# Optimization experiments

Measured on AMD Instinct MI355X. Metric: run time of the kernel, lower is better.

## Reference

```python
import jax, jax.numpy as jnp
import numpy as np

B, NQ, NV, DIM, HEADS, K = 2, 2048, 2048, 256, 8, 8
HD = DIM // HEADS
HID = 4 * DIM
SCALE = HD ** -0.5
EPS = 1e-5


def setup_inputs() -> dict:
    key = jax.random.key(0)
    ks = jax.random.split(key, 40)
    r = lambda i, s: jax.random.normal(ks[i], s, jnp.float32) * 0.02
    inp = {
        'q': jax.random.normal(ks[0], (B, NQ, DIM), jnp.float32),
        'v': jax.random.normal(ks[1], (B, NV, DIM), jnp.float32),
        'q_pos': jax.random.normal(ks[2], (B, NQ, 3), jnp.float32),
        'v_pos': jax.random.normal(ks[3], (B, NV, 3), jnp.float32),
        'self_knn_index': jax.random.randint(ks[4], (B, NQ, K), 0, NQ, jnp.int32),
        'cross_knn_index': jax.random.randint(ks[5], (B, NQ, K), 0, NV, jnp.int32),
        # LayerNorms (gamma=1, beta=0)
        'norm1_g': jnp.ones(DIM), 'norm1_b': jnp.zeros(DIM),
        'normq_g': jnp.ones(DIM), 'normq_b': jnp.zeros(DIM),
        'normv_g': jnp.ones(DIM), 'normv_b': jnp.zeros(DIM),
        'norm2_g': jnp.ones(DIM), 'norm2_b': jnp.zeros(DIM),
        # self-attention (qkv_bias=False), proj has bias
        'sa_qkv_w': r(6, (DIM, 3 * DIM)),
        'sa_proj_w': r(7, (DIM, DIM)), 'sa_proj_b': jnp.zeros(DIM),
        # cross-attention: q proj and kv proj (no bias), out proj with bias
        'ca_q_w': r(8, (DIM, DIM)),
        'ca_kv_w': r(9, (DIM, 2 * DIM)),
        'ca_proj_w': r(10, (DIM, DIM)), 'ca_proj_b': jnp.zeros(DIM),
        # MLP
        'fc1_w': r(11, (DIM, HID)), 'fc1_b': jnp.zeros(HID),
        'fc2_w': r(12, (HID, DIM)), 'fc2_b': jnp.zeros(DIM),
        # kNN maps
        'knn_w': r(13, (2 * DIM, DIM)), 'knn_b': jnp.zeros(DIM),
        'merge_w': r(14, (2 * DIM, DIM)), 'merge_b': jnp.zeros(DIM),
        'knnx_w': r(15, (2 * DIM, DIM)), 'knnx_b': jnp.zeros(DIM),
        'mergex_w': r(16, (2 * DIM, DIM)), 'mergex_b': jnp.zeros(DIM),
    }
    return inp


def _ln(x, g, b):
    m = x.mean(-1, keepdims=True)
    var = x.var(-1, keepdims=True)
    return (x - m) / jnp.sqrt(var + EPS) * g + b


def _heads(x):  # [B,N,DIM] -> [B,H,N,HD]
    Bx, N, _ = x.shape
    return x.reshape(Bx, N, HEADS, HD).transpose(0, 2, 1, 3)


def _attend(qh, kh, vh, proj_w, proj_b):
    a = jax.nn.softmax(jnp.einsum('bhqd,bhkd->bhqk', qh, kh) * SCALE, axis=-1)
    o = jnp.einsum('bhqk,bhkd->bhqd', a, vh)
    Bx, _, N, _ = o.shape
    o = o.transpose(0, 2, 1, 3).reshape(Bx, N, DIM)
    return o @ proj_w + proj_b


_gather = jax.vmap(lambda pts, idx: pts[idx])  # ([N,D],[Nq,K]) -> [Nq,K,D]


def _knn_feature(qn, vn, idx):  # gather -> diff/cat -> [B,Nq,K,2D]
    local = _gather(vn, idx)                      # [B,Nq,K,D]
    qe = qn[:, :, None, :]                        # [B,Nq,1,D]
    return jnp.concatenate([local - qe, jnp.broadcast_to(qe, local.shape)], -1)


def reference(q, v, q_pos, v_pos, self_knn_index, cross_knn_index,
              norm1_g, norm1_b, normq_g, normq_b, normv_g, normv_b,
              norm2_g, norm2_b, sa_qkv_w, sa_proj_w, sa_proj_b,
              ca_q_w, ca_kv_w, ca_proj_w, ca_proj_b,
              fc1_w, fc1_b, fc2_w, fc2_b,
              knn_w, knn_b, merge_w, merge_b,
              knnx_w, knnx_b, mergex_w, mergex_b):
    # ---- self-attention block with self-kNN branch ----
    nq = _ln(q, norm1_g, norm1_b)
    qkv = nq @ sa_qkv_w
    qh, kh, vh = (_heads(t) for t in jnp.split(qkv, 3, axis=-1))
    sa_out = _attend(qh, kh, vh, sa_proj_w, sa_proj_b)
    f = _knn_feature(nq, nq, self_knn_index)
    knn_out = jax.nn.leaky_relu(f @ knn_w + knn_b, 0.2).max(axis=-2)
    q1 = jnp.concatenate([sa_out, knn_out], -1) @ merge_w + merge_b
    q = q + q1
    # ---- cross-attention block with cross-kNN branch ----
    nq2 = _ln(q, normq_g, normq_b)
    nv = _ln(v, normv_g, normv_b)
    qh = _heads(nq2 @ ca_q_w)
    kh, vh = (_heads(t) for t in jnp.split(nv @ ca_kv_w, 2, axis=-1))
    ca_out = _attend(qh, kh, vh, ca_proj_w, ca_proj_b)
    f = _knn_feature(nq2, nv, cross_knn_index)
    knnx_out = jax.nn.leaky_relu(f @ knnx_w + knnx_b, 0.2).max(axis=-2)
    q2 = jnp.concatenate([ca_out, knnx_out], -1) @ mergex_w + mergex_b
    q = q + q2
    # ---- MLP block ----
    h = _ln(q, norm2_g, norm2_b)
    h = jax.nn.gelu(h @ fc1_w + fc1_b, approximate=False)
    q = q + (h @ fc2_w + fc2_b)
    return q
```

## Files before the change

### kernel.cpp

```cpp
#include <hip/hip_runtime.h>
#include <math.h>

#define NQC   2048
#define NKVC  2048
#define DIMC  256
#define SCALEF 0.2550348810731232f

typedef short bfrag __attribute__((ext_vector_type(8)));
typedef float ffrag __attribute__((ext_vector_type(4)));
typedef unsigned short us8 __attribute__((ext_vector_type(8)));

__device__ __forceinline__ float gelu_exact(float x) {
    return 0.5f * x * (1.0f + erff(x * 0.70710678118654752f));
}
__device__ __forceinline__ unsigned short f2bf(float f) {
    union { float f; unsigned u; } v; v.f = f;
    unsigned r = v.u + 0x7FFFu + ((v.u >> 16) & 1u);
    return (unsigned short)(r >> 16);
}
__device__ __forceinline__ float bf2f(unsigned short u) {
    union { unsigned u; float f; } v; v.u = ((unsigned)u) << 16;
    return v.f;
}
__device__ __forceinline__ float fexp2(float x) {
    float r; asm("v_exp_f32 %0, %1" : "=v"(r) : "v"(x)); return r;
}
__device__ __forceinline__ unsigned cvt_pk_bf16(float lo, float hi) {
    unsigned r; asm("v_cvt_pk_bf16_f32 %0, %1, %2" : "=v"(r) : "v"(lo), "v"(hi));
    return r;
}

__device__ __forceinline__ void ln_row(
    const float* __restrict__ x, const float* __restrict__ g,
    const float* __restrict__ b, unsigned short* __restrict__ y, int row)
{
    int lane = threadIdx.x & 63;
    const float* xr = x + (size_t)row * DIMC + lane * 4;
    float4 vv = *(const float4*)xr;
    float s  = vv.x + vv.y + vv.z + vv.w;
    float sq = vv.x*vv.x + vv.y*vv.y + vv.z*vv.z + vv.w*vv.w;
    #pragma unroll
    for (int off = 32; off >= 1; off >>= 1) {
        s  += __shfl_xor(s, off);
        sq += __shfl_xor(sq, off);
    }
    float mean = s * (1.0f/DIMC);
    float inv  = rsqrtf(sq * (1.0f/DIMC) - mean*mean + 1e-5f);
    float4 gg = *(const float4*)(g + lane*4);
    float4 bb = *(const float4*)(b + lane*4);
    ushort4 o;
    o.x = f2bf((vv.x - mean) * inv * gg.x + bb.x);
    o.y = f2bf((vv.y - mean) * inv * gg.y + bb.y);
    o.z = f2bf((vv.z - mean) * inv * gg.z + bb.z);
    o.w = f2bf((vv.w - mean) * inv * gg.w + bb.w);
    *(ushort4*)(y + (size_t)row * DIMC + lane * 4) = o;
}

__global__ __launch_bounds__(256) void prep_w(
    const float* __restrict__ qkv, const float* __restrict__ knn,
    const float* __restrict__ proj, const float* __restrict__ merge,
    const float* __restrict__ caq, const float* __restrict__ knnx,
    const float* __restrict__ cakv, const float* __restrict__ projx,
    const float* __restrict__ mergex, const float* __restrict__ fc1,
    const float* __restrict__ fc2, unsigned short* __restrict__ dst,
    const float* __restrict__ lx, const float* __restrict__ lg,
    const float* __restrict__ lb, unsigned short* __restrict__ ly,
    const float* __restrict__ vx, const float* __restrict__ vg,
    const float* __restrict__ vb, unsigned short* __restrict__ vy,
    const float* __restrict__ pb1, const float* __restrict__ mb1, float* __restrict__ bf1o,
    const float* __restrict__ pbx, const float* __restrict__ mbx, float* __restrict__ bfxo)
{
    __shared__ unsigned short T[64][72];
    int blk = blockIdx.x, tid = threadIdx.x;
    if (blk >= 2528) {
        const float* bp = (blk == 2528) ? pb1 : pbx;
        const float* Wm = (blk == 2528) ? merge : mergex;
        const float* bm = (blk == 2528) ? mb1 : mbx;
        float* o        = (blk == 2528) ? bf1o : bfxo;
        int m = tid;
        float acc = bm[m];
        for (int k = 0; k < 256; ++k) acc += bp[k] * Wm[(size_t)k * 256 + m];
        o[m] = acc;
        return;
    }
    if (blk >= 1504) {
        ln_row(vx, vg, vb, vy, (blk - 1504) * 4 + (tid >> 6));
        return;
    }
    if (blk >= 480) {
        ln_row(lx, lg, lb, ly, (blk - 480) * 4 + (tid >> 6));
        return;
    }
    if (blk >= 352) {
        int l = blk - 352;
        const float* s; unsigned short* d;
        if (l < 64) { s = proj;  d = dst + 327680; }
        else        { s = projx; d = dst + 851968; l -= 64; }
        int e = (l * 256 + tid) * 4;
        float4 v = *(const float4*)(s + e);
        ushort4 o;
        o.x = f2bf(v.x); o.y = f2bf(v.y); o.z = f2bf(v.z); o.w = f2bf(v.w);
        *(ushort4*)(d + e) = o;
        return;
    }
    int t = blk;
    const float* src; const float* src2 = nullptr; int sN;
    unsigned short* dp; int dK; float scale = 1.0f; int n0, k0;
    if (t < 48)       { src = qkv;          sN = 768;  dp = dst;           dK = 256;
                        n0 = (t % 12) * 64; k0 = (t / 12) * 64; if (n0 < 256) scale = SCALEF; }
    else if (t < 64)  { int u = t - 48;  src = knn;          sN = 256; dp = dst + 196608; dK = 256;
                        n0 = (u & 3) * 64; k0 = (u >> 2) * 64; }
    else if (t < 80)  { int u = t - 64;  src = knn + 65536;  src2 = knn; sN = 256; dp = dst + 262144; dK = 256;
                        n0 = (u & 3) * 64; k0 = (u >> 2) * 64; }
    else if (t < 112) { int u = t - 80;  src = merge;        sN = 256; dp = dst + 393216; dK = 512;
                        n0 = (u & 3) * 64; k0 = (u >> 2) * 64; }
    else if (t < 128) { int u = t - 112; src = caq;          sN = 256; dp = dst + 524288; dK = 256;
                        n0 = (u & 3) * 64; k0 = (u >> 2) * 64; scale = SCALEF; }
    else if (t < 144) { int u = t - 128; src = knnx + 65536; src2 = knnx; sN = 256; dp = dst + 589824; dK = 256;
                        n0 = (u & 3) * 64; k0 = (u >> 2) * 64; }
    else if (t < 176) { int u = t - 144; src = cakv;         sN = 512; dp = dst + 655360; dK = 256;
                        n0 = (u & 7) * 64; k0 = (u >> 3) * 64; }
    else if (t < 192) { int u = t - 176; src = knnx;         sN = 256; dp = dst + 786432; dK = 256;
                        n0 = (u & 3) * 64; k0 = (u >> 2) * 64; }
    else if (t < 224) { int u = t - 192; src = mergex;       sN = 256; dp = dst + 917504; dK = 512;
                        n0 = (u & 3) * 64; k0 = (u >> 2) * 64; }
    else if (t < 288) { int u = t - 224; src = fc1;          sN = 1024; dp = dst + 1048576; dK = 256;
                        n0 = (u & 15) * 64; k0 = (u >> 4) * 64; }
    else              { int u = t - 288; src = fc2;          sN = 256; dp = dst + 1310720; dK = 1024;
                        n0 = (u & 3) * 64; k0 = (u >> 2) * 64; }
    int r = tid >> 2, c0 = (tid & 3) * 16;
    float va[16];
    {
        const float* sp = src + (size_t)(k0 + r) * sN + n0 + c0;
        float4 f0 = *(const float4*)(sp);
        float4 f1 = *(const float4*)(sp + 4);
        float4 f2 = *(const float4*)(sp + 8);
        float4 f3 = *(const float4*)(sp + 12);
        va[0]=f0.x; va[1]=f0.y; va[2]=f0.z;  va[3]=f0.w;
        va[4]=f1.x; va[5]=f1.y; va[6]=f1.z;  va[7]=f1.w;
        va[8]=f2.x; va[9]=f2.y; va[10]=f2.z; va[11]=f2.w;
        va[12]=f3.x; va[13]=f3.y; va[14]=f3.z; va[15]=f3.w;
        if (src2) {
            const float* s2 = src2 + (size_t)(k0 + r) * sN + n0 + c0;
            float4 h0 = *(const float4*)(s2);
            float4 h1 = *(const float4*)(s2 + 4);
            float4 h2 = *(const float4*)(s2 + 8);
            float4 h3 = *(const float4*)(s2 + 12);
            va[0]-=h0.x; va[1]-=h0.y; va[2]-=h0.z;  va[3]-=h0.w;
            va[4]-=h1.x; va[5]-=h1.y; va[6]-=h1.z;  va[7]-=h1.w;
            va[8]-=h2.x; va[9]-=h2.y; va[10]-=h2.z; va[11]-=h2.w;
            va[12]-=h3.x; va[13]-=h3.y; va[14]-=h3.z; va[15]-=h3.w;
        }
    }
    #pragma unroll
    for (int i = 0; i < 16; ++i) T[c0 + i][r] = f2bf(va[i] * scale);
    __syncthreads();
    {
        int n = tid >> 2, kk = (tid & 3) * 16;
        unsigned short* d = dp + (size_t)(n0 + n) * dK + k0 + kk;
        *(us8*)d       = *(const us8*)&T[n][kk];
        *(us8*)(d + 8) = *(const us8*)&T[n][kk + 8];
    }
}

__global__ __launch_bounds__(256) void ln_b(
    const float* __restrict__ x, const float* __restrict__ g,
    const float* __restrict__ b, unsigned short* __restrict__ y)
{
    ln_row(x, g, b, y, blockIdx.x * 4 + (threadIdx.x >> 6));
}

template<int ACT, int RESID, int OUTBF>
__device__ __forceinline__ void gemm_body(
    const unsigned short* __restrict__ A, int lda,
    const unsigned short* __restrict__ Wt,
    const float* __restrict__ bias,
    const float* __restrict__ resid, int ldr,
    void* __restrict__ Cp, int ldc, int Kc, int row0, int col0,
    unsigned short (* __restrict__ Alds)[72],
    unsigned short (* __restrict__ Wlds)[72])
{
    const int tid = threadIdx.x;
    const int wid = tid >> 6, lane = tid & 63;
    const int lm = lane & 15, quad = lane >> 4;
    const int wr = wid >> 1, wc = wid & 1;
    const int ar = tid >> 2, ac = (tid & 3) * 16;
    const unsigned short* Ag = A  + (size_t)(row0 + ar) * lda + ac;
    const unsigned short* Wg = Wt + (size_t)(col0 + ar) * Kc  + ac;

    us8 a0 = *(const us8*)Ag;
    us8 a1 = *(const us8*)(Ag + 8);
    us8 w0 = *(const us8*)Wg;
    us8 w1 = *(const us8*)(Wg + 8);

    ffrag acc[2][2];
    #pragma unroll
    for (int mi = 0; mi < 2; ++mi)
        #pragma unroll
        for (int ni = 0; ni < 2; ++ni)
            acc[mi][ni] = (ffrag){0.f, 0.f, 0.f, 0.f};

    for (int k0 = 0;;) {
        __syncthreads();
        *(us8*)&Alds[ar][ac]   = a0;
        *(us8*)&Alds[ar][ac+8] = a1;
        *(us8*)&Wlds[ar][ac]   = w0;
        *(us8*)&Wlds[ar][ac+8] = w1;
        __syncthreads();
        k0 += 64;
        if (k0 < Kc) {
            a0 = *(const us8*)(Ag + k0);
            a1 = *(const us8*)(Ag + k0 + 8);
            w0 = *(const us8*)(Wg + k0);
            w1 = *(const us8*)(Wg + k0 + 8);
        }
        #pragma unroll
        for (int kc = 0; kc < 2; ++kc) {
            bfrag af[2], bw[2];
            #pragma unroll
            for (int mi = 0; mi < 2; ++mi)
                af[mi] = *(const bfrag*)&Alds[wr*32 + mi*16 + lm][kc*32 + quad*8];
            #pragma unroll
            for (int ni = 0; ni < 2; ++ni)
                bw[ni] = *(const bfrag*)&Wlds[wc*32 + ni*16 + lm][kc*32 + quad*8];
            #pragma unroll
            for (int mi = 0; mi < 2; ++mi)
                #pragma unroll
                for (int ni = 0; ni < 2; ++ni)
                    acc[mi][ni] = __builtin_amdgcn_mfma_f32_16x16x32_bf16(
                        af[mi], bw[ni], acc[mi][ni], 0, 0, 0);
        }
        if (k0 >= Kc) break;
    }
    #pragma unroll
    for (int mi = 0; mi < 2; ++mi) {
        #pragma unroll
        for (int ni = 0; ni < 2; ++ni) {
            int gr = row0 + wr*32 + mi*16 + quad*4;
            int gc = col0 + wc*32 + ni*16 + lm;
            float bv = bias ? bias[gc] : 0.f;
            #pragma unroll
            for (int r = 0; r < 4; ++r) {
                float o = acc[mi][ni][r] + bv;
                if (ACT == 1) o = gelu_exact(o);
                if (RESID) o += resid[(size_t)(gr + r) * ldr + gc];
                if (OUTBF) ((unsigned short*)Cp)[(size_t)(gr + r) * ldc + gc] = f2bf(o);
                else       ((float*)Cp)[(size_t)(gr + r) * ldc + gc] = o;
            }
        }
    }
}

template<int ACT, int RESID, int OUTBF>
__global__ __launch_bounds__(256) void gemm64(
    const unsigned short* __restrict__ A, int lda,
    const unsigned short* __restrict__ Wt,
    const float* __restrict__ bias,
    const float* __restrict__ resid, int ldr,
    void* __restrict__ Cp, int ldc, int Kc)
{
    __shared__ unsigned short Alds[64][72];
    __shared__ unsigned short Wlds[64][72];
    gemm_body<ACT,RESID,OUTBF>(A, lda, Wt, bias, resid, ldr, Cp, ldc, Kc,
                               blockIdx.y * 64, blockIdx.x * 64, Alds, Wlds);
}

__global__ __launch_bounds__(256) void gemm_qkv_fold(
    const unsigned short* __restrict__ XB, const unsigned short* __restrict__ WT1,
    unsigned short* __restrict__ A1,
    const unsigned short* __restrict__ WTmerge, const unsigned short* __restrict__ projbf,
    unsigned short* __restrict__ WTf1,
    const unsigned short* __restrict__ WTmergex, const unsigned short* __restrict__ projxbf,
    unsigned short* __restrict__ WTfx)
{
    __shared__ unsigned short Alds[64][72];
    __shared__ unsigned short Wlds[64][72];
    const unsigned short *A, *Wt; unsigned short* C;
    int lda, ldc, row0, col0;
    if (blockIdx.y >= 64) {
        if (blockIdx.x >= 16) return;
        row0 = (blockIdx.x >> 2) * 64; col0 = (blockIdx.x & 3) * 64;
        lda = 512; ldc = 256;
        if (blockIdx.y == 64) { A = WTmerge;  Wt = projbf;  C = WTf1; }
        else                  { A = WTmergex; Wt = projxbf; C = WTfx; }
    } else {
        A = XB; Wt = WT1; C = A1; lda = 256; ldc = 1280;
        row0 = blockIdx.y * 64; col0 = blockIdx.x * 64;
    }
    gemm_body<0,0,1>(A, lda, Wt, nullptr, nullptr, 0, C, ldc, 256, row0, col0, Alds, Wlds);
}

template<int ACT, int RESID, int OUTBF>
__global__ __launch_bounds__(512) void gemm64x8(
    const unsigned short* __restrict__ A, int lda,
    const unsigned short* __restrict__ Wt,
    const float* __restrict__ bias,
    const float* __restrict__ resid, int ldr,
    void* __restrict__ Cp, int ldc, int Kc)
{
    __shared__ unsigned short Alds[2][64][72];
    __shared__ unsigned short Wlds[2][64][72];
    __shared__ float Red[64][68];
    const int tid = threadIdx.x;
    const int g = tid >> 8;
    const int t = tid & 255;
    const int wid2 = (tid >> 6) & 3, lane = tid & 63;
    const int lm = lane & 15, quad = lane >> 4;
    const int wr = wid2 >> 1, wc = wid2 & 1;
    const int row0 = blockIdx.y * 64, col0 = blockIdx.x * 64;
    const int ar = t >> 2, ac = (t & 3) * 16;
    const int KH = Kc >> 1;
    const unsigned short* Ag = A  + (size_t)(row0 + ar) * lda + g * KH + ac;
    const unsigned short* Wg = Wt + (size_t)(col0 + ar) * Kc  + g * KH + ac;

    us8 a0 = *(const us8*)Ag;
    us8 a1 = *(const us8*)(Ag + 8);
    us8 w0 = *(const us8*)Wg;
    us8 w1 = *(const us8*)(Wg + 8);

    ffrag acc[2][2];
    #pragma unroll
    for (int mi = 0; mi < 2; ++mi)
        #pragma unroll
        for (int ni = 0; ni < 2; ++ni)
            acc[mi][ni] = (ffrag){0.f, 0.f, 0.f, 0.f};

    for (int k0 = 0;;) {
        __syncthreads();
        *(us8*)&Alds[g][ar][ac]   = a0;
        *(us8*)&Alds[g][ar][ac+8] = a1;
        *(us8*)&Wlds[g][ar][ac]   = w0;
        *(us8*)&Wlds[g][ar][ac+8] = w1;
        __syncthreads();
        k0 += 64;
        if (k0 < KH) {
            a0 = *(const us8*)(Ag + k0);
            a1 = *(const us8*)(Ag + k0 + 8);
            w0 = *(const us8*)(Wg + k0);
            w1 = *(const us8*)(Wg + k0 + 8);
        }
        #pragma unroll
        for (int kc = 0; kc < 2; ++kc) {
            bfrag af[2], bw[2];
            #pragma unroll
            for (int mi = 0; mi < 2; ++mi)
                af[mi] = *(const bfrag*)&Alds[g][wr*32 + mi*16 + lm][kc*32 + quad*8];
            #pragma unroll
            for (int ni = 0; ni < 2; ++ni)
                bw[ni] = *(const bfrag*)&Wlds[g][wc*32 + ni*16 + lm][kc*32 + quad*8];
            #pragma unroll
            for (int mi = 0; mi < 2; ++mi)
                #pragma unroll
                for (int ni = 0; ni < 2; ++ni)
                    acc[mi][ni] = __builtin_amdgcn_mfma_f32_16x16x32_bf16(
                        af[mi], bw[ni], acc[mi][ni], 0, 0, 0);
        }
        if (k0 >= KH) break;
    }
    __syncthreads();
    if (g == 1) {
        #pragma unroll
        for (int mi = 0; mi < 2; ++mi)
            #pragma unroll
            for (int ni = 0; ni < 2; ++ni) {
                int lr = wr*32 + mi*16 + quad*4;
                int lc = wc*32 + ni*16 + lm;
                #pragma unroll
                for (int r = 0; r < 4; ++r)
                    Red[lr + r][lc] = acc[mi][ni][r];
            }
    }
    __syncthreads();
    if (g == 0) {
        #pragma unroll
        for (int mi = 0; mi < 2; ++mi) {
            #pragma unroll
            for (int ni = 0; ni < 2; ++ni) {
                int lr = wr*32 + mi*16 + quad*4;
                int lc = wc*32 + ni*16 + lm;
                int gr = row0 + lr;
                int gc = col0 + lc;
                float bv = bias ? bias[gc] : 0.f;
                #pragma unroll
                for (int r = 0; r < 4; ++r) {
                    float o = acc[mi][ni][r] + Red[lr + r][lc] + bv;
                    if (ACT == 1) o = gelu_exact(o);
                    if (RESID) o += resid[(size_t)(gr + r) * ldr + gc];
                    if (OUTBF) ((unsigned short*)Cp)[(size_t)(gr + r) * ldc + gc] = f2bf(o);
                    else       ((float*)Cp)[(size_t)(gr + r) * ldc + gc] = o;
                }
            }
        }
    }
}

__global__ __launch_bounds__(512) void gemm64x8f(
    const unsigned short* __restrict__ Op, const float* __restrict__ Lp,
    const unsigned short* __restrict__ Akn,
    const unsigned short* __restrict__ Wat,
    const unsigned short* __restrict__ Wkn,
    const float* __restrict__ bias,
    const float* __restrict__ resid,
    float* __restrict__ Cp)
{
    __shared__ unsigned short Alds[2][64][72];
    __shared__ unsigned short Wlds[2][64][72];
    __shared__ float Red[64][68];
    const int tid = threadIdx.x;
    const int g = tid >> 8;
    const int t = tid & 255;
    const int wid2 = (tid >> 6) & 3, lane = tid & 63;
    const int lm = lane & 15, quad = lane >> 4;
    const int wr = wid2 >> 1, wc = wid2 & 1;
    const int row0 = blockIdx.y * 64, col0 = blockIdx.x * 64;
    const int ar = t >> 2, ac = (t & 3) * 16;
    const int grow = row0 + ar;

    const unsigned short* O0 = Op + (size_t)grow * 256 + ac;
    const unsigned short* O1 = Op + (size_t)(4096 + grow) * 256 + ac;
    const float* L0 = Lp + (size_t)grow * 8;
    const float* L1 = Lp + (size_t)(4096 + grow) * 8;
    const unsigned short* Ak = Akn + (size_t)grow * 512 + ac;
    const unsigned short* Wg = g ? Wkn + (size_t)(col0 + ar) * 512 + ac
                                 : Wat + (size_t)(col0 + ar) * 256 + ac;

    us8 a0, a1, o10, o11;
    float li = 0.f;
    if (g == 0) {
        a0  = *(const us8*)O0;  a1  = *(const us8*)(O0 + 8);
        o10 = *(const us8*)O1;  o11 = *(const us8*)(O1 + 8);
        li  = 1.0f / (L0[ac >> 5] + L1[ac >> 5]);
    } else {
        a0 = *(const us8*)Ak;   a1 = *(const us8*)(Ak + 8);
    }
    us8 w0 = *(const us8*)Wg;
    us8 w1 = *(const us8*)(Wg + 8);

    ffrag acc[2][2];
    #pragma unroll
    for (int mi = 0; mi < 2; ++mi)
        #pragma unroll
        for (int ni = 0; ni < 2; ++ni)
            acc[mi][ni] = (ffrag){0.f, 0.f, 0.f, 0.f};

    for (int k0 = 0;;) {
        us8 s0 = a0, s1 = a1;
        if (g == 0) {
            #pragma unroll
            for (int i = 0; i < 8; ++i) {
                s0[i] = f2bf((bf2f(a0[i]) + bf2f(o10[i])) * li);
                s1[i] = f2bf((bf2f(a1[i]) + bf2f(o11[i])) * li);
            }
        }
        __syncthreads();
        *(us8*)&Alds[g][ar][ac]   = s0;
        *(us8*)&Alds[g][ar][ac+8] = s1;
        *(us8*)&Wlds[g][ar][ac]   = w0;
        *(us8*)&Wlds[g][ar][ac+8] = w1;
        __syncthreads();
        k0 += 64;
        if (k0 < 256) {
            if (g == 0) {
                a0  = *(const us8*)(O0 + k0);  a1  = *(const us8*)(O0 + k0 + 8);
                o10 = *(const us8*)(O1 + k0);  o11 = *(const us8*)(O1 + k0 + 8);
                li  = 1.0f / (L0[(k0 + ac) >> 5] + L1[(k0 + ac) >> 5]);
            } else {
                a0 = *(const us8*)(Ak + k0);   a1 = *(const us8*)(Ak + k0 + 8);
            }
            w0 = *(const us8*)(Wg + k0);
            w1 = *(const us8*)(Wg + k0 + 8);
        }
        #pragma unroll
        for (int kc = 0; kc < 2; ++kc) {
            bfrag af[2], bw[2];
            #pragma unroll
            for (int mi = 0; mi < 2; ++mi)
                af[mi] = *(const bfrag*)&Alds[g][wr*32 + mi*16 + lm][kc*32 + quad*8];
            #pragma unroll
            for (int ni = 0; ni < 2; ++ni)
                bw[ni] = *(const bfrag*)&Wlds[g][wc*32 + ni*16 + lm][kc*32 + quad*8];
            #pragma unroll
            for (int mi = 0; mi < 2; ++mi)
                #pragma unroll
                for (int ni = 0; ni < 2; ++ni)
                    acc[mi][ni] = __builtin_amdgcn_mfma_f32_16x16x32_bf16(
                        af[mi], bw[ni], acc[mi][ni], 0, 0, 0);
        }
        if (k0 >= 256) break;
    }
    __syncthreads();
    if (g == 1) {
        #pragma unroll
        for (int mi = 0; mi < 2; ++mi)
            #pragma unroll
            for (int ni = 0; ni < 2; ++ni) {
                int lr = wr*32 + mi*16 + quad*4;
                int lc = wc*32 + ni*16 + lm;
                #pragma unroll
                for (int r = 0; r < 4; ++r)
                    Red[lr + r][lc] = acc[mi][ni][r];
            }
    }
    __syncthreads();
    if (g == 0) {
        #pragma unroll
        for (int mi = 0; mi < 2; ++mi) {
            #pragma unroll
            for (int ni = 0; ni < 2; ++ni) {
                int lr = wr*32 + mi*16 + quad*4;
                int lc = wc*32 + ni*16 + lm;
                int gr = row0 + lr;
                int gc = col0 + lc;
                float bv = bias[gc];
                #pragma unroll
                for (int r = 0; r < 4; ++r)
                    Cp[(size_t)(gr + r) * 256 + gc] =
                        acc[mi][ni][r] + Red[lr + r][lc] + bv
                        + resid[(size_t)(gr + r) * 256 + gc];
            }
        }
    }
}

__global__ __launch_bounds__(256) void gemm64_dual(
    const unsigned short* __restrict__ XB,
    const unsigned short* __restrict__ NVB,
    const unsigned short* __restrict__ WT2,
    const unsigned short* __restrict__ WT3,
    unsigned short* __restrict__ A2,
    unsigned short* __restrict__ A3)
{
    __shared__ unsigned short Alds[64][72];
    __shared__ unsigned short Wlds[64][72];
    const unsigned short* A; const unsigned short* Wt;
    unsigned short* C; int ldc, col0;
    if (blockIdx.x < 8) { A = XB;  Wt = WT2; C = A2; ldc = 512; col0 = blockIdx.x * 64; }
    else                { A = NVB; Wt = WT3; C = A3; ldc = 768; col0 = (blockIdx.x - 8) * 64; }
    gemm_body<0,0,1>(A, 256, Wt, nullptr, nullptr, 0, C, ldc, 256,
                     blockIdx.y * 64, col0, Alds, Wlds);
}

__global__ __launch_bounds__(256) void attn_gather(
    const unsigned short* __restrict__ Qp, int ldq,
    const unsigned short* __restrict__ Kp, int ldk,
    const unsigned short* __restrict__ Vp, int ldv,
    unsigned short* __restrict__ Op, float* __restrict__ Lp,
    const unsigned short* __restrict__ P, int ldp,
    const unsigned short* __restrict__ Base, int ldb,
    const float* __restrict__ gbias, const int* __restrict__ idx,
    unsigned short* __restrict__ gout, int ldgo)
{
    __shared__ unsigned short Klds[64][40];
    __shared__ __align__(16) unsigned short Vt[32][72];
    __shared__ __align__(16) unsigned short Plds[4][16][72];
    int tid = threadIdx.x, wid = tid >> 6, lane = tid & 63;

    if (blockIdx.z >= 4) {
        int gbid = blockIdx.x + 32 * (blockIdx.y + 8 * (blockIdx.z - 4));
        int q = gbid * 4 + wid;
        int b = q >> 11;
        int c = lane * 4;
        ushort4 bu = *(const ushort4*)(Base + (size_t)q * ldb + c);
        float4 bi = *(const float4*)(gbias + c);
        float bsx = bf2f(bu.x) + bi.x, bsy = bf2f(bu.y) + bi.y;
        float bsz = bf2f(bu.z) + bi.z, bsw = bf2f(bu.w) + bi.w;
        float4 acc = make_float4(-3e38f, -3e38f, -3e38f, -3e38f);
        const int* ip = idx + (size_t)q * 8;
        #pragma unroll
        for (int k = 0; k < 8; ++k) {
            int j = ip[k];
            ushort4 pu = *(const ushort4*)(P + ((size_t)(b * NKVC + j)) * ldp + c);
            float t;
            t = bsx + bf2f(pu.x); t = t > 0.f ? t : 0.2f * t; acc.x = fmaxf(acc.x, t);
            t = bsy + bf2f(pu.y); t = t > 0.f ? t : 0.2f * t; acc.y = fmaxf(acc.y, t);
            t = bsz + bf2f(pu.z); t = t > 0.f ? t : 0.2f * t; acc.z = fmaxf(acc.z, t);
            t = bsw + bf2f(pu.w); t = t > 0.f ? t : 0.2f * t; acc.w = fmaxf(acc.w, t);
        }
        ushort4 o;
        o.x = f2bf(acc.x); o.y = f2bf(acc.y); o.z = f2bf(acc.z); o.w = f2bf(acc.w);
        *(ushort4*)(gout + (size_t)q * ldgo + c) = o;
        return;
    }

    int zc = blockIdx.z, bb = zc >> 1, ck = zc & 1;
    int h = blockIdx.y;
    int hoff = h * 32;
    int lm = lane & 15, quad = lane >> 4;
    size_t qbase  = (size_t)bb * NQC;
    size_t kvbase = (size_t)bb * NKVC;
    int q0 = blockIdx.x * 64 + wid * 16;

    bfrag aq = *(const bfrag*)(Qp + (qbase + q0 + lm) * (size_t)ldq + hoff + quad * 8);

    float l_r[4] = {0.f, 0.f, 0.f, 0.f};
    ffrag oacc[2];
    oacc[0] = (ffrag){0.f, 0.f, 0.f, 0.f};
    oacc[1] = (ffrag){0.f, 0.f, 0.f, 0.f};

    const int kkey = tid >> 2, kd0 = (tid & 3) * 8;
    const int vkey = tid & 63, vd0 = (tid >> 6) * 8;
    const int vcol = ((vkey & 15) << 2) | (vkey >> 4);
    const unsigned short* kg0 = Kp + (kvbase + kkey) * (size_t)ldk + hoff + kd0;
    const unsigned short* vg0 = Vp + (kvbase + vkey) * (size_t)ldv + hoff + vd0;

    for (int kt = ck * 16; kt < ck * 16 + 16; ++kt) {
        us8 kv = *(const us8*)(kg0 + (size_t)kt * 64 * ldk);
        us8 vv = *(const us8*)(vg0 + (size_t)kt * 64 * ldv);
        __syncthreads();
        *(us8*)&Klds[kkey][kd0] = kv;
        #pragma unroll
        for (int i = 0; i < 8; ++i) Vt[vd0 + i][vcol] = vv[i];
        __syncthreads();

        ffrag sacc[4];
        #pragma unroll
        for (int t = 0; t < 4; ++t) {
            bfrag bk = *(const bfrag*)&Klds[t*16 + lm][quad * 8];
            sacc[t] = __builtin_amdgcn_mfma_f32_16x16x32_bf16(
                aq, bk, (ffrag){0.f,0.f,0.f,0.f}, 0, 0, 0);
        }

        #pragma unroll
        for (int r = 0; r < 4; ++r) {
            float p0 = fexp2(sacc[0][r]), p1 = fexp2(sacc[1][r]);
            float p2 = fexp2(sacc[2][r]), p3 = fexp2(sacc[3][r]);
            l_r[r] += (p0 + p1) + (p2 + p3);
            unsigned u0 = cvt_pk_bf16(p0, p1);
            unsigned u1 = cvt_pk_bf16(p2, p3);
            *(uint2*)&Plds[wid][quad*4 + r][lm << 2] = make_uint2(u0, u1);
        }
        asm volatile("s_waitcnt lgkmcnt(0)" ::: "memory");

        #pragma unroll
        for (int kc = 0; kc < 2; ++kc) {
            bfrag ap = *(const bfrag*)&Plds[wid][lm][kc*32 + quad*8];
            #pragma unroll
            for (int nt = 0; nt < 2; ++nt) {
                bfrag bv = *(const bfrag*)&Vt[nt*16 + lm][kc*32 + quad*8];
                oacc[nt] = __builtin_amdgcn_mfma_f32_16x16x32_bf16(
                    ap, bv, oacc[nt], 0, 0, 0);
            }
        }
    }
    #pragma unroll
    for (int nt = 0; nt < 2; ++nt)
        #pragma unroll
        for (int r = 0; r < 4; ++r)
            Op[((size_t)ck * 4096 + qbase + q0 + quad*4 + r) * 256 + hoff + nt*16 + lm]
                = f2bf(oacc[nt][r]);
    #pragma unroll
    for (int r = 0; r < 4; ++r) {
        float l = l_r[r];
        l += __shfl_xor(l, 1);
        l += __shfl_xor(l, 2);
        l += __shfl_xor(l, 4);
        l += __shfl_xor(l, 8);
        if (lm == 0)
            Lp[((size_t)ck * 4096 + qbase + q0 + quad*4 + r) * 8 + h] = l;
    }
}

extern "C" void kernel_launch(void* const* d_in, const int* in_sizes, int n_in,
                              void* d_out, int out_size, void* d_ws, size_t ws_size,
                              hipStream_t stream) {
    const float* q_in   = (const float*)d_in[0];
    const float* v_in   = (const float*)d_in[1];
    const int*   idx_s  = (const int*)d_in[4];
    const int*   idx_x  = (const int*)d_in[5];
    const float* n1g = (const float*)d_in[6],  *n1b = (const float*)d_in[7];
    const float* nqg = (const float*)d_in[8],  *nqb = (const float*)d_in[9];
    const float* nvg = (const float*)d_in[10], *nvb = (const float*)d_in[11];
    const float* n2g = (const float*)d_in[12], *n2b = (const float*)d_in[13];
    const float* sa_qkv_w  = (const float*)d_in[14];
    const float* sa_proj_w = (const float*)d_in[15];
    const float* sa_proj_b = (const float*)d_in[16];
    const float* ca_q_w    = (const float*)d_in[17];
    const float* ca_kv_w   = (const float*)d_in[18];
    const float* ca_proj_w = (const float*)d_in[19];
    const float* ca_proj_b = (const float*)d_in[20];
    const float* fc1_w = (const float*)d_in[21], *fc1_b = (const float*)d_in[22];
    const float* fc2_w = (const float*)d_in[23], *fc2_b = (const float*)d_in[24];
    const float* knn_w   = (const float*)d_in[25], *knn_b   = (const float*)d_in[26];
    const float* merge_w = (const float*)d_in[27], *merge_b = (const float*)d_in[28];
    const float* knnx_w  = (const float*)d_in[29], *knnx_b  = (const float*)d_in[30];
    const float* mergex_w = (const float*)d_in[31], *mergex_b = (const float*)d_in[32];
    float* out = (float*)d_out;

    unsigned short* A1      = (unsigned short*)d_ws;
    unsigned short* A2      = A1;
    unsigned short* A3      = A1 + (size_t)4096 * 512;
    unsigned short* Hb      = A1;
    unsigned short* KN      = A1 + (size_t)4096 * 1280;
    unsigned short* CC      = KN;
    unsigned short* XB      = CC + (size_t)4096 * 512;
    unsigned short* NVB     = XB + (size_t)4096 * 256;
    unsigned short* WT      = NVB + (size_t)4096 * 256;
    unsigned short* WT1     = WT;
    unsigned short* projbf  = WT + 327680;
    unsigned short* WTmerge = WT + 393216;
    unsigned short* WT2     = WT + 524288;
    unsigned short* WT3     = WT + 655360;
    unsigned short* projxbf = WT + 851968;
    unsigned short* WTmergex= WT + 917504;
    unsigned short* WTfc1   = WT + 1048576;
    unsigned short* WTfc2   = WT + 1310720;
    unsigned short* Opart   = WT + 1572864;
    float* Lpart = (float*)(Opart + (size_t)2 * 4096 * 256);
    unsigned short* WTf1 = (unsigned short*)(Lpart + (size_t)2 * 4096 * 8);
    unsigned short* WTfx = WTf1 + 65536;
    float* bf1 = (float*)(WTfx + 65536);
    float* bfx = bf1 + 256;

    dim3 blk(256), blk8(512);
    dim3 gAG(NQC / 64, 8, 8);

    prep_w<<<dim3(2530), blk, 0, stream>>>(sa_qkv_w, knn_w, sa_proj_w, merge_w,
        ca_q_w, knnx_w, ca_kv_w, ca_proj_w, mergex_w, fc1_w, fc2_w, WT,
        q_in, n1g, n1b, XB,
        v_in, nvg, nvb, NVB,
        sa_proj_b, merge_b, bf1,
        ca_proj_b, mergex_b, bfx);

    gemm_qkv_fold<<<dim3(20,66), blk, 0, stream>>>(XB, WT1, A1,
        WTmerge, projbf, WTf1, WTmergex, projxbf, WTfx);
    attn_gather<<<gAG, blk, 0, stream>>>(A1, 1280, A1+256, 1280, A1+512, 1280,
        Opart, Lpart, A1+768, 1280, A1+1024, 1280, knn_b, idx_s, CC+256, 512);
    gemm64x8f<<<dim3(4,64), blk8, 0, stream>>>(Opart, Lpart, CC+256,
        WTf1, WTmerge+256, bf1, q_in, out);

    ln_b<<<dim3(1024), blk, 0, stream>>>(out, nqg, nqb, XB);
    gemm64_dual<<<dim3(20,64), blk, 0, stream>>>(XB, NVB, WT2, WT3, A2, A3);
    attn_gather<<<gAG, blk, 0, stream>>>(A2, 512, A3, 768, A3+256, 768,
        Opart, Lpart, A3+512, 768, A2+256, 512, knnx_b, idx_x, CC+256, 512);
    gemm64x8f<<<dim3(4,64), blk8, 0, stream>>>(Opart, Lpart, CC+256,
        WTfx, WTmergex+256, bfx, out, out);

    ln_b<<<dim3(1024), blk, 0, stream>>>(out, n2g, n2b, XB);
    gemm64<1,0,1><<<dim3(16,64), blk, 0, stream>>>(XB, 256, WTfc1,
        fc1_b, nullptr, 0, Hb, 1024, 256);
    gemm64x8<0,1,0><<<dim3(4,64), blk8, 0, stream>>>(Hb, 1024, WTfc2,
        fc2_b, out, 256, out, 256, 1024);
}
```

Before: 236.9 us.

## Fuse merge GEMM with following LayerNorm using full-row 16-row tiles

Replaces the 64x64-tile merge GEMM (split-K across two 256-thread groups with a shared-memory reduction) and the separate LayerNorm kernel with one kernel. Each block now computes 16 full output rows across all 256 columns and runs K=512 serially, then applies LayerNorm in-block and writes the bf16 normalized output. This removes a launch and the re-read of the fp32 output for LN. In exchange the grid shrinks to 256 blocks, each block reloads the full weight matrix, and per-block K work doubles, which lowers parallelism and weight reuse.

```diff
diff --git a/kernel.cpp b/kernel.cpp
--- a/kernel.cpp
+++ b/kernel.cpp
@@ -163,13 +163,6 @@
     }
 }
 
-__global__ __launch_bounds__(256) void ln_b(
-    const float* __restrict__ x, const float* __restrict__ g,
-    const float* __restrict__ b, unsigned short* __restrict__ y)
-{
-    ln_row(x, g, b, y, blockIdx.x * 4 + (threadIdx.x >> 6));
-}
-
 template<int ACT, int RESID, int OUTBF>
 __device__ __forceinline__ void gemm_body(
     const unsigned short* __restrict__ A, int lda,
@@ -394,131 +387,126 @@
     }
 }
 
-__global__ __launch_bounds__(512) void gemm64x8f(
+__global__ __launch_bounds__(512) void gemm_mln(
     const unsigned short* __restrict__ Op, const float* __restrict__ Lp,
     const unsigned short* __restrict__ Akn,
     const unsigned short* __restrict__ Wat,
     const unsigned short* __restrict__ Wkn,
     const float* __restrict__ bias,
     const float* __restrict__ resid,
-    float* __restrict__ Cp)
-{
-    __shared__ unsigned short Alds[2][64][72];
-    __shared__ unsigned short Wlds[2][64][72];
-    __shared__ float Red[64][68];
+    float* __restrict__ Cp,
+    const float* __restrict__ lng, const float* __restrict__ lnb,
+    unsigned short* __restrict__ ln_out)
+{
+    __shared__ unsigned short Wlds[256][72];
+    __shared__ unsigned short Alds[16][72];
+    __shared__ float OutT[16][268];
     const int tid = threadIdx.x;
-    const int g = tid >> 8;
-    const int t = tid & 255;
-    const int wid2 = (tid >> 6) & 3, lane = tid & 63;
+    const int wid = tid >> 6, lane = tid & 63;
     const int lm = lane & 15, quad = lane >> 4;
-    const int wr = wid2 >> 1, wc = wid2 & 1;
-    const int row0 = blockIdx.y * 64, col0 = blockIdx.x * 64;
-    const int ar = t >> 2, ac = (t & 3) * 16;
-    const int grow = row0 + ar;
-
-    const unsigned short* O0 = Op + (size_t)grow * 256 + ac;
-    const unsigned short* O1 = Op + (size_t)(4096 + grow) * 256 + ac;
-    const float* L0 = Lp + (size_t)grow * 8;
-    const float* L1 = Lp + (size_t)(4096 + grow) * 8;
-    const unsigned short* Ak = Akn + (size_t)grow * 512 + ac;
-    const unsigned short* Wg = g ? Wkn + (size_t)(col0 + ar) * 512 + ac
-                                 : Wat + (size_t)(col0 + ar) * 256 + ac;
-
-    us8 a0, a1, o10, o11;
-    float li = 0.f;
-    if (g == 0) {
-        a0  = *(const us8*)O0;  a1  = *(const us8*)(O0 + 8);
-        o10 = *(const us8*)O1;  o11 = *(const us8*)(O1 + 8);
-        li  = 1.0f / (L0[ac >> 5] + L1[ac >> 5]);
-    } else {
-        a0 = *(const us8*)Ak;   a1 = *(const us8*)(Ak + 8);
-    }
-    us8 w0 = *(const us8*)Wg;
-    us8 w1 = *(const us8*)(Wg + 8);
-
-    ffrag acc[2][2];
-    #pragma unroll
-    for (int mi = 0; mi < 2; ++mi)
-        #pragma unroll
-        for (int ni = 0; ni < 2; ++ni)
-            acc[mi][ni] = (ffrag){0.f, 0.f, 0.f, 0.f};
+    const int row0 = blockIdx.x * 16;
+    const int wn = tid >> 1, wk = (tid & 1) * 32;
+    const int ar = tid >> 3, ac = (tid & 7) * 8;
+
+    const unsigned short* O0 = Op + (size_t)(row0 + ar) * 256 + ac;
+    const unsigned short* O1 = Op + (size_t)(4096 + row0 + ar) * 256 + ac;
+    const float* L0 = Lp + (size_t)(row0 + ar) * 8;
+    const float* L1 = Lp + (size_t)(4096 + row0 + ar) * 8;
+    const unsigned short* Ak = Akn + (size_t)(row0 + ar) * 512 + ac;
+
+    us8 aReg, wv0, wv1, wv2, wv3;
+    if (tid < 128) {
+        us8 x = *(const us8*)O0;
+        us8 y = *(const us8*)O1;
+        float li = 1.0f / (L0[ac >> 5] + L1[ac >> 5]);
+        #pragma unroll
+        for (int i = 0; i < 8; ++i)
+            aReg[i] = f2bf((bf2f(x[i]) + bf2f(y[i])) * li);
+    }
+    {
+        const unsigned short* Wg = Wat + (size_t)wn * 256 + wk;
+        wv0 = *(const us8*)Wg;        wv1 = *(const us8*)(Wg + 8);
+        wv2 = *(const us8*)(Wg + 16); wv3 = *(const us8*)(Wg + 24);
+    }
+
+    ffrag acc[2];
+    acc[0] = (ffrag){0.f, 0.f, 0.f, 0.f};
+    acc[1] = (ffrag){0.f, 0.f, 0.f, 0.f};
 
     for (int k0 = 0;;) {
-        us8 s0 = a0, s1 = a1;
-        if (g == 0) {
-            #pragma unroll
-            for (int i = 0; i < 8; ++i) {
-                s0[i] = f2bf((bf2f(a0[i]) + bf2f(o10[i])) * li);
-                s1[i] = f2bf((bf2f(a1[i]) + bf2f(o11[i])) * li);
-            }
-        }
         __syncthreads();
-        *(us8*)&Alds[g][ar][ac]   = s0;
-        *(us8*)&Alds[g][ar][ac+8] = s1;
-        *(us8*)&Wlds[g][ar][ac]   = w0;
-        *(us8*)&Wlds[g][ar][ac+8] = w1;
+        if (tid < 128) *(us8*)&Alds[ar][ac] = aReg;
+        *(us8*)&Wlds[wn][wk]      = wv0;
+        *(us8*)&Wlds[wn][wk + 8]  = wv1;
+        *(us8*)&Wlds[wn][wk + 16] = wv2;
+        *(us8*)&Wlds[wn][wk + 24] = wv3;
         __syncthreads();
         k0 += 64;
-        if (k0 < 256) {
-            if (g == 0) {
-                a0  = *(const us8*)(O0 + k0);  a1  = *(const us8*)(O0 + k0 + 8);
-                o10 = *(const us8*)(O1 + k0);  o11 = *(const us8*)(O1 + k0 + 8);
-                li  = 1.0f / (L0[(k0 + ac) >> 5] + L1[(k0 + ac) >> 5]);
-            } else {
-                a0 = *(const us8*)(Ak + k0);   a1 = *(const us8*)(Ak + k0 + 8);
+        if (k0 < 512) {
+            if (tid < 128) {
+                if (k0 < 256) {
+                    us8 x = *(const us8*)(O0 + k0);
+                    us8 y = *(const us8*)(O1 + k0);
+                    float li = 1.0f / (L0[(k0 + ac) >> 5] + L1[(k0 + ac) >> 5]);
+                    #pragma unroll
+                    for (int i = 0; i < 8; ++i)
+                        aReg[i] = f2bf((bf2f(x[i]) + bf2f(y[i])) * li);
+                } else {
+                    aReg = *(const us8*)(Ak + (k0 - 256));
+                }
             }
-            w0 = *(const us8*)(Wg + k0);
-            w1 = *(const us8*)(Wg + k0 + 8);
+            const unsigned short* Wg = (k0 < 256)
+                ? Wat + (size_t)wn * 256 + k0 + wk
+                : Wkn + (size_t)wn * 512 + (k0 - 256) + wk;
+            wv0 = *(const us8*)Wg;        wv1 = *(const us8*)(Wg + 8);
+            wv2 = *(const us8*)(Wg + 16); wv3 = *(const us8*)(Wg + 24);
         }
         #pragma unroll
         for (int kc = 0; kc < 2; ++kc) {
-            bfrag af[2], bw[2];
-            #pragma unroll
-            for (int mi = 0; mi < 2; ++mi)
-                af[mi] = *(const bfrag*)&Alds[g][wr*32 + mi*16 + lm][kc*32 + quad*8];
-            #pragma unroll
-            for (int ni = 0; ni < 2; ++ni)
-                bw[ni] = *(const bfrag*)&Wlds[g][wc*32 + ni*16 + lm][kc*32 + quad*8];
-            #pragma unroll
-            for (int mi = 0; mi < 2; ++mi)
-                #pragma unroll
-                for (int ni = 0; ni < 2; ++ni)
-                    acc[mi][ni] = __builtin_amdgcn_mfma_f32_16x16x32_bf16(
-                        af[mi], bw[ni], acc[mi][ni], 0, 0, 0);
-        }
-        if (k0 >= 256) break;
+            bfrag af = *(const bfrag*)&Alds[lm][kc*32 + quad*8];
+            #pragma unroll
+            for (int ni = 0; ni < 2; ++ni) {
+                bfrag bw = *(const bfrag*)&Wlds[wid*32 + ni*16 + lm][kc*32 + quad*8];
+                acc[ni] = __builtin_amdgcn_mfma_f32_16x16x32_bf16(
+                    af, bw, acc[ni], 0, 0, 0);
+            }
+        }
+        if (k0 >= 512) break;
+    }
+    #pragma unroll
+    for (int ni = 0; ni < 2; ++ni) {
+        int gc = wid*32 + ni*16 + lm;
+        float bv = bias[gc];
+        #pragma unroll
+        for (int r = 0; r < 4; ++r) {
+            int lr = quad*4 + r;
+            float o = acc[ni][r] + bv + resid[(size_t)(row0 + lr) * 256 + gc];
+            Cp[(size_t)(row0 + lr) * 256 + gc] = o;
+            OutT[lr][gc] = o;
+        }
     }
     __syncthreads();
-    if (g == 1) {
-        #pragma unroll
-        for (int mi = 0; mi < 2; ++mi)
-            #pragma unroll
-            for (int ni = 0; ni < 2; ++ni) {
-                int lr = wr*32 + mi*16 + quad*4;
-                int lc = wc*32 + ni*16 + lm;
-                #pragma unroll
-                for (int r = 0; r < 4; ++r)
-                    Red[lr + r][lc] = acc[mi][ni][r];
-            }
-    }
-    __syncthreads();
-    if (g == 0) {
-        #pragma unroll
-        for (int mi = 0; mi < 2; ++mi) {
-            #pragma unroll
-            for (int ni = 0; ni < 2; ++ni) {
-                int lr = wr*32 + mi*16 + quad*4;
-                int lc = wc*32 + ni*16 + lm;
-                int gr = row0 + lr;
-                int gc = col0 + lc;
-                float bv = bias[gc];
-                #pragma unroll
-                for (int r = 0; r < 4; ++r)
-                    Cp[(size_t)(gr + r) * 256 + gc] =
-                        acc[mi][ni][r] + Red[lr + r][lc] + bv
-                        + resid[(size_t)(gr + r) * 256 + gc];
-            }
-        }
+    #pragma unroll
+    for (int rr0 = 0; rr0 < 2; ++rr0) {
+        int rr = wid * 2 + rr0;
+        float4 vv = *(const float4*)&OutT[rr][lane * 4];
+        float s  = vv.x + vv.y + vv.z + vv.w;
+        float sq = vv.x*vv.x + vv.y*vv.y + vv.z*vv.z + vv.w*vv.w;
+        #pragma unroll
+        for (int off = 32; off >= 1; off >>= 1) {
+            s  += __shfl_xor(s, off);
+            sq += __shfl_xor(sq, off);
+        }
+        float mean = s * (1.0f/DIMC);
+        float inv  = rsqrtf(sq * (1.0f/DIMC) - mean*mean + 1e-5f);
+        float4 gg = *(const float4*)(lng + lane*4);
+        float4 bb = *(const float4*)(lnb + lane*4);
+        ushort4 o;
+        o.x = f2bf((vv.x - mean) * inv * gg.x + bb.x);
+        o.y = f2bf((vv.y - mean) * inv * gg.y + bb.y);
+        o.z = f2bf((vv.z - mean) * inv * gg.z + bb.z);
+        o.w = f2bf((vv.w - mean) * inv * gg.w + bb.w);
+        *(ushort4*)(ln_out + (size_t)(row0 + rr) * 256 + lane * 4) = o;
     }
 }
 
@@ -725,17 +713,15 @@
         WTmerge, projbf, WTf1, WTmergex, projxbf, WTfx);
     attn_gather<<<gAG, blk, 0, stream>>>(A1, 1280, A1+256, 1280, A1+512, 1280,
         Opart, Lpart, A1+768, 1280, A1+1024, 1280, knn_b, idx_s, CC+256, 512);
-    gemm64x8f<<<dim3(4,64), blk8, 0, stream>>>(Opart, Lpart, CC+256,
-        WTf1, WTmerge+256, bf1, q_in, out);
-
-    ln_b<<<dim3(1024), blk, 0, stream>>>(out, nqg, nqb, XB);
+    gemm_mln<<<dim3(256), blk8, 0, stream>>>(Opart, Lpart, CC+256,
+        WTf1, WTmerge+256, bf1, q_in, out, nqg, nqb, XB);
+
     gemm64_dual<<<dim3(20,64), blk, 0, stream>>>(XB, NVB, WT2, WT3, A2, A3);
     attn_gather<<<gAG, blk, 0, stream>>>(A2, 512, A3, 768, A3+256, 768,
         Opart, Lpart, A3+512, 768, A2+256, 512, knnx_b, idx_x, CC+256, 512);
-    gemm64x8f<<<dim3(4,64), blk8, 0, stream>>>(Opart, Lpart, CC+256,
-        WTfx, WTmergex+256, bfx, out, out);
-
-    ln_b<<<dim3(1024), blk, 0, stream>>>(out, n2g, n2b, XB);
+    gemm_mln<<<dim3(256), blk8, 0, stream>>>(Opart, Lpart, CC+256,
+        WTfx, WTmergex+256, bfx, out, out, n2g, n2b, XB);
+
     gemm64<1,0,1><<<dim3(16,64), blk, 0, stream>>>(XB, 256, WTfc1,
         fc1_b, nullptr, 0, Hb, 1024, 256);
     gemm64x8<0,1,0><<<dim3(4,64), blk8, 0, stream>>>(Hb, 1024, WTfc2,
```

After: 235.6 us. About the same (-0.6%).
